# Optimization experiments

Hardware: AMD Instinct MI355X
Metric: run time of the kernel (lower is better)

The kernel has to match this reference:

```python
import jax, jax.numpy as jnp
import numpy as np
from jax import lax

B = 256; D_IN = 2048; HID = 2048; NSEG = 10; D_CTX = 1024; OUT = 100; NI = 205
KW_PCT = 0.05
K = int(round(KW_PCT * HID))  # 102 winners per sample per layer
W_DENSITY = 0.05      # weight_sparsity = 0.95
DEND_DENSITY = 0.05   # dendrite_weight_sparsity = 0.95


def setup_inputs() -> dict:
    key = jax.random.key(0)
    ks = jax.random.split(key, 16)
    def u(k, shape, bound):
        return jax.random.uniform(k, shape, minval=-bound, maxval=bound, dtype=jnp.float32)
    inp = {}
    inp["x"] = jax.random.normal(ks[0], (B, D_IN), jnp.float32)
    inp["context"] = jax.random.normal(ks[1], (B, D_CTX), jnp.float32)
    # layer 1 FF weights: modified kaiming, input density 1.0 -> bound = 1/sqrt(fan_in)
    inp["W1"] = u(ks[2], (HID, D_IN), 1.0 / np.sqrt(D_IN))
    inp["b1"] = jnp.zeros((HID,), jnp.float32)
    # dendrites: input density 1.0 (context_percent_on=1), weight density 0.05
    dend_bound = 1.0 / np.sqrt(DEND_DENSITY * D_CTX)
    inp["segW1"] = u(ks[3], (HID, NSEG, D_CTX), dend_bound)
    inp["maskW1"] = (jax.random.uniform(ks[4], (HID, D_IN)) < W_DENSITY).astype(jnp.float32)
    inp["maskS1"] = (jax.random.uniform(ks[5], (HID, NSEG, D_CTX)) < DEND_DENSITY).astype(jnp.float32)
    # layer 2 FF weights: input density = kw_percent_on (k-winners upstream)
    inp["W2"] = u(ks[6], (HID, HID), 1.0 / np.sqrt(KW_PCT * HID))
    inp["b2"] = jnp.zeros((HID,), jnp.float32)
    inp["segW2"] = u(ks[7], (HID, NSEG, D_CTX), dend_bound)
    inp["maskW2"] = (jax.random.uniform(ks[8], (HID, HID)) < W_DENSITY).astype(jnp.float32)
    inp["maskS2"] = (jax.random.uniform(ks[9], (HID, NSEG, D_CTX)) < DEND_DENSITY).astype(jnp.float32)
    # Dale (EiDense) output head: non-negative excitatory/inhibitory factors
    s = 1.0 / np.sqrt(HID)
    inp["Wex_out"] = jax.random.uniform(ks[10], (OUT, HID), dtype=jnp.float32) * s
    inp["Wix_out"] = jax.random.uniform(ks[11], (1, HID), dtype=jnp.float32) * s
    inp["Wei_out"] = jax.random.uniform(ks[12], (OUT, 1), dtype=jnp.float32)
    inp["b_out"] = jnp.zeros((OUT,), jnp.float32)
    return inp


def _kwinners(y, k):
    # keep top-k activations per row, zero the rest (boost_strength=0)
    vals, idxs = lax.top_k(y, k)  # [B, k]
    rows = jnp.arange(y.shape[0])[:, None]
    return jnp.zeros_like(y).at[rows, idxs].set(vals)


def _dendritic_layer(x, context, W, b, segW, maskW, maskS):
    # sparse-masked feedforward projection
    y = x @ (W * maskW).T + b  # [B, HID]
    # per-unit dendrite segment activations from context
    d = jnp.einsum('bc,usc->bus', context, segW * maskS)  # [B, HID, NSEG]
    # absolute-max gating: pick segment with max |activation|, gate by sigmoid
    sel = jnp.argmax(jnp.abs(d), axis=-1)  # [B, HID]
    chosen = jnp.take_along_axis(d, sel[..., None], axis=-1)[..., 0]
    y = y * jax.nn.sigmoid(chosen)
    return _kwinners(y, K)


def reference(x, context, W1, b1, segW1, maskW1, maskS1, W2, b2, segW2, maskW2, maskS2, Wex_out, Wix_out, Wei_out, b_out):
    h = _dendritic_layer(x, context, W1, b1, segW1, maskW1, maskS1)
    h = _dendritic_layer(h, context, W2, b2, segW2, maskW2, maskS2)
    # EiDense output head: W = Wex - Wei @ Wix (Dale's law), no output nonlinearity
    W_out = Wex_out - Wei_out @ Wix_out  # [OUT, HID]
    return h @ W_out.T + b_out
```

## Files before the change

### kernel.cpp

```cpp
#include <hip/hip_runtime.h>
#include <math.h>

#define B_SZ   256
#define D_IN   2048
#define HID    2048
#define NSEG   10
#define D_CTX  1024
#define OUT_N  100
#define KWIN   102
#define CAP    256

typedef float f32x4 __attribute__((ext_vector_type(4)));

__device__ __forceinline__ f32x4 ntld4(const float* p) {
  return __builtin_nontemporal_load((const f32x4*)p);
}

__device__ __forceinline__ unsigned f2key(float f) {
  unsigned b = __float_as_uint(f);
  return (b & 0x80000000u) ? ~b : (b | 0x80000000u);
}
__device__ __forceinline__ float key2f(unsigned k) {
  return (k & 0x80000000u) ? __uint_as_float(k & 0x7FFFFFFFu) : __uint_as_float(~k);
}

__global__ __launch_bounds__(256) void transpose_k(const float* __restrict__ src,
                                                   float* __restrict__ dst,
                                                   int rows, int cols) {
  __shared__ float tile[32][33];
  int c0 = blockIdx.x * 32, r0 = blockIdx.y * 32;
  int tx = threadIdx.x, ty = threadIdx.y;
  for (int i = ty; i < 32; i += 8)
    tile[i][tx] = src[(r0 + i) * cols + (c0 + tx)];
  __syncthreads();
  for (int i = ty; i < 32; i += 8)
    dst[(c0 + i) * rows + (r0 + tx)] = tile[tx][i];
}

__device__ __forceinline__ int compact_seg(const float* __restrict__ wrow,
                                           const float* __restrict__ mrow,
                                           int len4, float2* pairs, int* scnt) {
  const int t = threadIdx.x & 63;
  if (t == 0) *scnt = 0;
  __syncthreads();
  for (int e = t; e < len4; e += 64) {
    f32x4 w = ntld4(wrow + 4 * e);
    f32x4 m = ntld4(mrow + 4 * e);
    bool n0 = (m.x != 0.f), n1 = (m.y != 0.f), n2 = (m.z != 0.f), n3 = (m.w != 0.f);
    int nz = (int)n0 + (int)n1 + (int)n2 + (int)n3;
    if (nz) {
      int pos = atomicAdd(scnt, nz);
      int c = e << 2;
      if (n0) { if (pos < CAP) pairs[pos] = make_float2(w.x, __int_as_float(c));     pos++; }
      if (n1) { if (pos < CAP) pairs[pos] = make_float2(w.y, __int_as_float(c + 1)); pos++; }
      if (n2) { if (pos < CAP) pairs[pos] = make_float2(w.z, __int_as_float(c + 2)); pos++; }
      if (n3) { if (pos < CAP) pairs[pos] = make_float2(w.w, __int_as_float(c + 3)); pos++; }
    }
  }
  __syncthreads();
  int c = *scnt;
  return c > CAP ? CAP : c;
}

__device__ __forceinline__ void gather_dot(const float* __restrict__ src,
                                           const float2* pairs, int cnt,
                                           int t4, float out4[4]) {
  float acc[4][4];
#pragma unroll
  for (int s = 0; s < 4; ++s)
#pragma unroll
    for (int i = 0; i < 4; ++i) acc[s][i] = 0.f;
  int j = 0;
  for (; j + 8 <= cnt; j += 8) {
#pragma unroll
    for (int s = 0; s < 8; ++s) {
      float2 p = pairs[j + s];
      const f32x4 cv = *(const f32x4*)(src + (__float_as_int(p.y) << 8) + t4);
      acc[s & 3][0] += cv.x * p.x; acc[s & 3][1] += cv.y * p.x;
      acc[s & 3][2] += cv.z * p.x; acc[s & 3][3] += cv.w * p.x;
    }
  }
  for (; j < cnt; ++j) {
    float2 p = pairs[j];
    const f32x4 cv = *(const f32x4*)(src + (__float_as_int(p.y) << 8) + t4);
    acc[0][0] += cv.x * p.x; acc[0][1] += cv.y * p.x;
    acc[0][2] += cv.z * p.x; acc[0][3] += cv.w * p.x;
  }
#pragma unroll
  for (int i = 0; i < 4; ++i)
    out4[i] = (acc[0][i] + acc[1][i]) + (acc[2][i] + acc[3][i]);
}

__global__ __launch_bounds__(256, 4) void dend_kernel(
    const float* __restrict__ W1, const float* __restrict__ maskW1, const float* __restrict__ b1,
    const float* __restrict__ segW1, const float* __restrict__ maskS1,
    const float* __restrict__ segW2, const float* __restrict__ maskS2,
    const float* __restrict__ xT, const float* __restrict__ ctxT,
    float* __restrict__ y1T, float* __restrict__ gate2T) {
  __shared__ float2 pairs_s[4][CAP];
  __shared__ int scnt_s[4];
  const int wave = threadIdx.x >> 6;
  const int t = threadIdx.x & 63, t4 = t * 4;
  float2* pairs = pairs_s[wave];
  int* scnt = &scnt_s[wave];
  const int row = blockIdx.x * 4 + wave;

  float bestA[4] = {-1.f, -1.f, -1.f, -1.f};
  float chosen[4] = {0.f, 0.f, 0.f, 0.f};

  if (row < HID) {
    const int u = row;
    int cnt = compact_seg(W1 + u * D_IN, maskW1 + u * D_IN, D_IN / 4, pairs, scnt);
    float ff[4];
    gather_dot(xT, pairs, cnt, t4, ff);
    for (int s = 0; s < NSEG; ++s) {
      const int r = (u * NSEG + s) * D_CTX;
      cnt = compact_seg(segW1 + r, maskS1 + r, D_CTX / 4, pairs, scnt);
      float d[4];
      gather_dot(ctxT, pairs, cnt, t4, d);
#pragma unroll
      for (int i = 0; i < 4; ++i) {
        float a = fabsf(d[i]);
        if (a > bestA[i]) { bestA[i] = a; chosen[i] = d[i]; }
      }
    }
    float bb = b1[u];
    float4 o;
    o.x = (ff[0] + bb) / (1.f + expf(-chosen[0]));
    o.y = (ff[1] + bb) / (1.f + expf(-chosen[1]));
    o.z = (ff[2] + bb) / (1.f + expf(-chosen[2]));
    o.w = (ff[3] + bb) / (1.f + expf(-chosen[3]));
    *(float4*)(y1T + u * B_SZ + t4) = o;
  } else {
    const int u = row - HID;
    for (int s = 0; s < NSEG; ++s) {
      const int r = (u * NSEG + s) * D_CTX;
      int cnt = compact_seg(segW2 + r, maskS2 + r, D_CTX / 4, pairs, scnt);
      float d[4];
      gather_dot(ctxT, pairs, cnt, t4, d);
#pragma unroll
      for (int i = 0; i < 4; ++i) {
        float a = fabsf(d[i]);
        if (a > bestA[i]) { bestA[i] = a; chosen[i] = d[i]; }
      }
    }
    float4 g;
    g.x = 1.f / (1.f + expf(-chosen[0]));
    g.y = 1.f / (1.f + expf(-chosen[1]));
    g.z = 1.f / (1.f + expf(-chosen[2]));
    g.w = 1.f / (1.f + expf(-chosen[3]));
    *(float4*)(gate2T + u * B_SZ + t4) = g;
  }
}

__global__ __launch_bounds__(256, 4) void ff2_kernel(
    const float* __restrict__ W2, const float* __restrict__ maskW2, const float* __restrict__ b2,
    const float* __restrict__ h1T, const float* __restrict__ gate2T, float* __restrict__ y2T) {
  __shared__ float2 pairs_s[4][CAP];
  __shared__ int scnt_s[4];
  const int wave = threadIdx.x >> 6;
  const int t = threadIdx.x & 63, t4 = t * 4;
  const int u = blockIdx.x * 4 + wave;
  int cnt = compact_seg(W2 + u * HID, maskW2 + u * HID, HID / 4, pairs_s[wave], &scnt_s[wave]);
  float acc[4];
  gather_dot(h1T, pairs_s[wave], cnt, t4, acc);
  float bb = b2[u];
  float4 g = *(const float4*)(gate2T + u * B_SZ + t4);
  float4 o;
  o.x = (acc[0] + bb) * g.x; o.y = (acc[1] + bb) * g.y;
  o.z = (acc[2] + bb) * g.z; o.w = (acc[3] + bb) * g.w;
  *(float4*)(y2T + u * B_SZ + t4) = o;
}

__global__ __launch_bounds__(256) void topk_kernel(float* __restrict__ y) {
  const int b = blockIdx.x, t = threadIdx.x;
  __shared__ int hist[256];
  __shared__ int sfx[256];
  __shared__ unsigned sPref;
  __shared__ int sRem;
  float* __restrict__ row = y + b * HID;
  unsigned myk[8];
  f32x4 v0 = *(const f32x4*)(row + t * 8);
  f32x4 v1 = *(const f32x4*)(row + t * 8 + 4);
  myk[0] = f2key(v0.x); myk[1] = f2key(v0.y); myk[2] = f2key(v0.z); myk[3] = f2key(v0.w);
  myk[4] = f2key(v1.x); myk[5] = f2key(v1.y); myk[6] = f2key(v1.z); myk[7] = f2key(v1.w);
  unsigned pref = 0;
  int rem = KWIN;
  for (int shift = 24; shift >= 0; shift -= 8) {
    hist[t] = 0;
    __syncthreads();
    unsigned hiMask = (shift == 24) ? 0u : (0xFFFFFFFFu << (shift + 8));
#pragma unroll
    for (int i = 0; i < 8; ++i) {
      unsigned k = myk[i];
      if ((k & hiMask) == pref) atomicAdd(&hist[(k >> shift) & 255], 1);
    }
    __syncthreads();
    sfx[t] = hist[t];
    __syncthreads();
    for (int off = 1; off < 256; off <<= 1) {
      int add = (t + off < 256) ? sfx[t + off] : 0;
      __syncthreads();
      sfx[t] += add;
      __syncthreads();
    }
    int s_incl = sfx[t];
    int s_excl = (t == 255) ? 0 : sfx[t + 1];
    if (s_incl >= rem && s_excl < rem) {
      sPref = pref | (((unsigned)t) << shift);
      sRem = rem - s_excl;
    }
    __syncthreads();
    pref = sPref;
    rem = sRem;
    __syncthreads();
  }
  int eq = 0;
#pragma unroll
  for (int i = 0; i < 8; ++i) eq += (myk[i] == pref) ? 1 : 0;
  sfx[t] = eq;
  __syncthreads();
  for (int off = 1; off < 256; off <<= 1) {
    int add = (t >= off) ? sfx[t - off] : 0;
    __syncthreads();
    sfx[t] += add;
    __syncthreads();
  }
  int excl = sfx[t] - eq;
  int taken = 0;
  float o[8];
#pragma unroll
  for (int i = 0; i < 8; ++i) {
    unsigned k = myk[i];
    bool keep;
    if (k > pref) keep = true;
    else if (k == pref) { keep = (excl + taken) < rem; taken++; }
    else keep = false;
    o[i] = keep ? key2f(k) : 0.f;
  }
  f32x4 w0 = {o[0], o[1], o[2], o[3]};
  f32x4 w1 = {o[4], o[5], o[6], o[7]};
  *(f32x4*)(row + t * 8) = w0;
  *(f32x4*)(row + t * 8 + 4) = w1;
}

__global__ __launch_bounds__(256) void out_kernel(
    const float* __restrict__ h2, const float* __restrict__ Wex, const float* __restrict__ Wix,
    const float* __restrict__ Wei, const float* __restrict__ bo, float* __restrict__ out) {
  const int b = blockIdx.x, t = threadIdx.x;
  __shared__ float hrow[HID];
  __shared__ float red[256];
  float part = 0.f;
#pragma unroll
  for (int i = 0; i < 8; ++i) {
    int u = t + 256 * i;
    float v = h2[b * HID + u];
    hrow[u] = v;
    part += v * Wix[u];
  }
  red[t] = part;
  __syncthreads();
  for (int off = 128; off > 0; off >>= 1) {
    if (t < off) red[t] += red[t + off];
    __syncthreads();
  }
  float S = red[0];
  const int w = t >> 6, l = t & 63;
  for (int o = w; o < OUT_N; o += 4) {
    float acc = 0.f;
    const float* wr = Wex + o * HID;
#pragma unroll
    for (int q = 0; q < HID / 64; ++q) acc += hrow[l + 64 * q] * wr[l + 64 * q];
    for (int off = 32; off > 0; off >>= 1) acc += __shfl_down(acc, off, 64);
    if (l == 0) out[b * OUT_N + o] = acc - Wei[o] * S + bo[o];
  }
}

extern "C" void kernel_launch(void* const* d_in, const int* in_sizes, int n_in,
                              void* d_out, int out_size, void* d_ws, size_t ws_size,
                              hipStream_t stream) {
  const float* x      = (const float*)d_in[0];
  const float* ctx    = (const float*)d_in[1];
  const float* W1     = (const float*)d_in[2];
  const float* b1     = (const float*)d_in[3];
  const float* segW1  = (const float*)d_in[4];
  const float* maskW1 = (const float*)d_in[5];
  const float* maskS1 = (const float*)d_in[6];
  const float* W2     = (const float*)d_in[7];
  const float* b2     = (const float*)d_in[8];
  const float* segW2  = (const float*)d_in[9];
  const float* maskW2 = (const float*)d_in[10];
  const float* maskS2 = (const float*)d_in[11];
  const float* Wex    = (const float*)d_in[12];
  const float* Wix    = (const float*)d_in[13];
  const float* Wei    = (const float*)d_in[14];
  const float* bo     = (const float*)d_in[15];
  float* out = (float*)d_out;
  float* ws = (float*)d_ws;

  float* xT     = ws;
  float* ctxT   = ws + 524288;
  float* y1T    = ws + 786432;
  float* bufA   = ws + 1310720;
  float* h1T    = ws + 1835008;
  float* gate2T = ws + 2359296;

  dim3 tb(32, 8);
  transpose_k<<<dim3(D_IN / 32, B_SZ / 32), tb, 0, stream>>>(x, xT, B_SZ, D_IN);
  transpose_k<<<dim3(D_CTX / 32, B_SZ / 32), tb, 0, stream>>>(ctx, ctxT, B_SZ, D_CTX);
  dend_kernel<<<2 * HID / 4, 256, 0, stream>>>(W1, maskW1, b1, segW1, maskS1, segW2, maskS2,
                                               xT, ctxT, y1T, gate2T);
  transpose_k<<<dim3(B_SZ / 32, HID / 32), tb, 0, stream>>>(y1T, bufA, HID, B_SZ);
  topk_kernel<<<B_SZ, 256, 0, stream>>>(bufA);
  transpose_k<<<dim3(HID / 32, B_SZ / 32), tb, 0, stream>>>(bufA, h1T, B_SZ, HID);
  ff2_kernel<<<HID / 4, 256, 0, stream>>>(W2, maskW2, b2, h1T, gate2T, y1T);
  transpose_k<<<dim3(B_SZ / 32, HID / 32), tb, 0, stream>>>(y1T, bufA, HID, B_SZ);
  topk_kernel<<<B_SZ, 256, 0, stream>>>(bufA);
  out_kernel<<<B_SZ, 256, 0, stream>>>(bufA, Wex, Wix, Wei, bo, out);
}
```

Before: 519.9 us.

## Prefetch dendrite segments into registers and fold transposes into top-k

The dendrite kernel now loads the next segment's weights and masks into registers while the current segment is gathered and dotted. This overlaps global-memory latency with compute, and occupancy is lowered to 3 blocks to make room for the extra registers. Per-wave compaction uses wave barriers instead of block-wide __syncthreads. The four intermediate transpose kernels are removed: top-k reads the transposed activations with strided accesses and writes either transposed or row-major output, and the two input transposes are merged into one launch. This cuts launches and round trips through intermediate buffers, at the cost of uncoalesced strided reads and writes in top-k.

```diff
diff --git a/kernel.cpp b/kernel.cpp
--- a/kernel.cpp
+++ b/kernel.cpp
@@ -24,25 +24,33 @@
   return (k & 0x80000000u) ? __uint_as_float(k & 0x7FFFFFFFu) : __uint_as_float(~k);
 }
 
-__global__ __launch_bounds__(256) void transpose_k(const float* __restrict__ src,
-                                                   float* __restrict__ dst,
-                                                   int rows, int cols) {
+__global__ __launch_bounds__(256) void transpose2_k(const float* __restrict__ xsrc,
+                                                    float* __restrict__ xdst,
+                                                    const float* __restrict__ csrc,
+                                                    float* __restrict__ cdst) {
   __shared__ float tile[32][33];
-  int c0 = blockIdx.x * 32, r0 = blockIdx.y * 32;
-  int tx = threadIdx.x, ty = threadIdx.y;
+  int bid = blockIdx.x;
+  const float* src; float* dst; int cols;
+  const int NX = (D_IN / 32) * (B_SZ / 32);
+  if (bid < NX) { src = xsrc; dst = xdst; cols = D_IN; }
+  else { bid -= NX; src = csrc; dst = cdst; cols = D_CTX; }
+  int nbx = cols / 32;
+  int bx = bid % nbx, by = bid / nbx;
+  int c0 = bx * 32, r0 = by * 32;
+  int tx = threadIdx.x & 31, ty = threadIdx.x >> 5;
   for (int i = ty; i < 32; i += 8)
     tile[i][tx] = src[(r0 + i) * cols + (c0 + tx)];
   __syncthreads();
   for (int i = ty; i < 32; i += 8)
-    dst[(c0 + i) * rows + (r0 + tx)] = tile[tx][i];
-}
-
-__device__ __forceinline__ int compact_seg(const float* __restrict__ wrow,
-                                           const float* __restrict__ mrow,
-                                           int len4, float2* pairs, int* scnt) {
+    dst[(c0 + i) * B_SZ + (r0 + tx)] = tile[tx][i];
+}
+
+__device__ __forceinline__ int compact_wave(const float* __restrict__ wrow,
+                                            const float* __restrict__ mrow,
+                                            int len4, float2* pairs, int* scnt) {
   const int t = threadIdx.x & 63;
   if (t == 0) *scnt = 0;
-  __syncthreads();
+  __builtin_amdgcn_wave_barrier();
   for (int e = t; e < len4; e += 64) {
     f32x4 w = ntld4(wrow + 4 * e);
     f32x4 m = ntld4(mrow + 4 * e);
@@ -57,9 +65,45 @@
       if (n3) { if (pos < CAP) pairs[pos] = make_float2(w.w, __int_as_float(c + 3)); pos++; }
     }
   }
-  __syncthreads();
+  __builtin_amdgcn_wave_barrier();
   int c = *scnt;
   return c > CAP ? CAP : c;
+}
+
+__device__ __forceinline__ int store_seg(const f32x4 w[4], const f32x4 m[4],
+                                         float2* pairs, int* scnt) {
+  const int t = threadIdx.x & 63;
+  if (t == 0) *scnt = 0;
+  __builtin_amdgcn_wave_barrier();
+#pragma unroll
+  for (int i = 0; i < 4; ++i) {
+    int e = t + 64 * i;
+    f32x4 ww = w[i], mm = m[i];
+    bool n0 = (mm.x != 0.f), n1 = (mm.y != 0.f), n2 = (mm.z != 0.f), n3 = (mm.w != 0.f);
+    int nz = (int)n0 + (int)n1 + (int)n2 + (int)n3;
+    if (nz) {
+      int pos = atomicAdd(scnt, nz);
+      int c = e << 2;
+      if (n0) { if (pos < CAP) pairs[pos] = make_float2(ww.x, __int_as_float(c));     pos++; }
+      if (n1) { if (pos < CAP) pairs[pos] = make_float2(ww.y, __int_as_float(c + 1)); pos++; }
+      if (n2) { if (pos < CAP) pairs[pos] = make_float2(ww.z, __int_as_float(c + 2)); pos++; }
+      if (n3) { if (pos < CAP) pairs[pos] = make_float2(ww.w, __int_as_float(c + 3)); pos++; }
+    }
+  }
+  __builtin_amdgcn_wave_barrier();
+  int c = *scnt;
+  return c > CAP ? CAP : c;
+}
+
+__device__ __forceinline__ void load_seg(const float* __restrict__ wrow,
+                                         const float* __restrict__ mrow,
+                                         f32x4 w[4], f32x4 m[4]) {
+  const int t = threadIdx.x & 63;
+#pragma unroll
+  for (int i = 0; i < 4; ++i) {
+    w[i] = ntld4(wrow + 4 * (t + 64 * i));
+    m[i] = ntld4(mrow + 4 * (t + 64 * i));
+  }
 }
 
 __device__ __forceinline__ void gather_dot(const float* __restrict__ src,
@@ -91,7 +135,7 @@
     out4[i] = (acc[0][i] + acc[1][i]) + (acc[2][i] + acc[3][i]);
 }
 
-__global__ __launch_bounds__(256, 4) void dend_kernel(
+__global__ __launch_bounds__(256, 3) void dend_kernel(
     const float* __restrict__ W1, const float* __restrict__ maskW1, const float* __restrict__ b1,
     const float* __restrict__ segW1, const float* __restrict__ maskS1,
     const float* __restrict__ segW2, const float* __restrict__ maskS2,
@@ -105,51 +149,53 @@
   int* scnt = &scnt_s[wave];
   const int row = blockIdx.x * 4 + wave;
 
+  const bool isL1 = (row < HID);
+  const int u = isL1 ? row : (row - HID);
+  const float* segW = (isL1 ? segW1 : segW2) + (size_t)u * NSEG * D_CTX;
+  const float* maskS = (isL1 ? maskS1 : maskS2) + (size_t)u * NSEG * D_CTX;
+
   float bestA[4] = {-1.f, -1.f, -1.f, -1.f};
   float chosen[4] = {0.f, 0.f, 0.f, 0.f};
-
-  if (row < HID) {
-    const int u = row;
-    int cnt = compact_seg(W1 + u * D_IN, maskW1 + u * D_IN, D_IN / 4, pairs, scnt);
-    float ff[4];
+  float ff[4] = {0.f, 0.f, 0.f, 0.f};
+
+  f32x4 w[4], m[4];
+  if (isL1) {
+    int cnt = compact_wave(W1 + (size_t)u * D_IN, maskW1 + (size_t)u * D_IN,
+                           D_IN / 4, pairs, scnt);
+    load_seg(segW, maskS, w, m);
     gather_dot(xT, pairs, cnt, t4, ff);
-    for (int s = 0; s < NSEG; ++s) {
-      const int r = (u * NSEG + s) * D_CTX;
-      cnt = compact_seg(segW1 + r, maskS1 + r, D_CTX / 4, pairs, scnt);
-      float d[4];
-      gather_dot(ctxT, pairs, cnt, t4, d);
-#pragma unroll
-      for (int i = 0; i < 4; ++i) {
-        float a = fabsf(d[i]);
-        if (a > bestA[i]) { bestA[i] = a; chosen[i] = d[i]; }
-      }
-    }
+  } else {
+    load_seg(segW, maskS, w, m);
+  }
+
+  for (int s = 0; s < NSEG; ++s) {
+    int cnt = store_seg(w, m, pairs, scnt);
+    if (s + 1 < NSEG)
+      load_seg(segW + (s + 1) * D_CTX, maskS + (s + 1) * D_CTX, w, m);
+    float d[4];
+    gather_dot(ctxT, pairs, cnt, t4, d);
+#pragma unroll
+    for (int i = 0; i < 4; ++i) {
+      float a = fabsf(d[i]);
+      if (a > bestA[i]) { bestA[i] = a; chosen[i] = d[i]; }
+    }
+  }
+
+  if (isL1) {
     float bb = b1[u];
     float4 o;
     o.x = (ff[0] + bb) / (1.f + expf(-chosen[0]));
     o.y = (ff[1] + bb) / (1.f + expf(-chosen[1]));
     o.z = (ff[2] + bb) / (1.f + expf(-chosen[2]));
     o.w = (ff[3] + bb) / (1.f + expf(-chosen[3]));
-    *(float4*)(y1T + u * B_SZ + t4) = o;
+    *(float4*)(y1T + (size_t)u * B_SZ + t4) = o;
   } else {
-    const int u = row - HID;
-    for (int s = 0; s < NSEG; ++s) {
-      const int r = (u * NSEG + s) * D_CTX;
-      int cnt = compact_seg(segW2 + r, maskS2 + r, D_CTX / 4, pairs, scnt);
-      float d[4];
-      gather_dot(ctxT, pairs, cnt, t4, d);
-#pragma unroll
-      for (int i = 0; i < 4; ++i) {
-        float a = fabsf(d[i]);
-        if (a > bestA[i]) { bestA[i] = a; chosen[i] = d[i]; }
-      }
-    }
     float4 g;
     g.x = 1.f / (1.f + expf(-chosen[0]));
     g.y = 1.f / (1.f + expf(-chosen[1]));
     g.z = 1.f / (1.f + expf(-chosen[2]));
     g.w = 1.f / (1.f + expf(-chosen[3]));
-    *(float4*)(gate2T + u * B_SZ + t4) = g;
+    *(float4*)(gate2T + (size_t)u * B_SZ + t4) = g;
   }
 }
 
@@ -161,29 +207,29 @@
   const int wave = threadIdx.x >> 6;
   const int t = threadIdx.x & 63, t4 = t * 4;
   const int u = blockIdx.x * 4 + wave;
-  int cnt = compact_seg(W2 + u * HID, maskW2 + u * HID, HID / 4, pairs_s[wave], &scnt_s[wave]);
+  int cnt = compact_wave(W2 + (size_t)u * HID, maskW2 + (size_t)u * HID,
+                         HID / 4, pairs_s[wave], &scnt_s[wave]);
   float acc[4];
   gather_dot(h1T, pairs_s[wave], cnt, t4, acc);
   float bb = b2[u];
-  float4 g = *(const float4*)(gate2T + u * B_SZ + t4);
+  float4 g = *(const float4*)(gate2T + (size_t)u * B_SZ + t4);
   float4 o;
   o.x = (acc[0] + bb) * g.x; o.y = (acc[1] + bb) * g.y;
   o.z = (acc[2] + bb) * g.z; o.w = (acc[3] + bb) * g.w;
-  *(float4*)(y2T + u * B_SZ + t4) = o;
-}
-
-__global__ __launch_bounds__(256) void topk_kernel(float* __restrict__ y) {
+  *(float4*)(y2T + (size_t)u * B_SZ + t4) = o;
+}
+
+__global__ __launch_bounds__(256) void topk_kernel(const float* __restrict__ yT,
+                                                   float* __restrict__ dst, int mode) {
   const int b = blockIdx.x, t = threadIdx.x;
   __shared__ int hist[256];
   __shared__ int sfx[256];
   __shared__ unsigned sPref;
   __shared__ int sRem;
-  float* __restrict__ row = y + b * HID;
   unsigned myk[8];
-  f32x4 v0 = *(const f32x4*)(row + t * 8);
-  f32x4 v1 = *(const f32x4*)(row + t * 8 + 4);
-  myk[0] = f2key(v0.x); myk[1] = f2key(v0.y); myk[2] = f2key(v0.z); myk[3] = f2key(v0.w);
-  myk[4] = f2key(v1.x); myk[5] = f2key(v1.y); myk[6] = f2key(v1.z); myk[7] = f2key(v1.w);
+#pragma unroll
+  for (int i = 0; i < 8; ++i)
+    myk[i] = f2key(yT[(size_t)(t * 8 + i) * B_SZ + b]);
   unsigned pref = 0;
   int rem = KWIN;
   for (int shift = 24; shift >= 0; shift -= 8) {
@@ -228,7 +274,6 @@
   }
   int excl = sfx[t] - eq;
   int taken = 0;
-  float o[8];
 #pragma unroll
   for (int i = 0; i < 8; ++i) {
     unsigned k = myk[i];
@@ -236,12 +281,11 @@
     if (k > pref) keep = true;
     else if (k == pref) { keep = (excl + taken) < rem; taken++; }
     else keep = false;
-    o[i] = keep ? key2f(k) : 0.f;
-  }
-  f32x4 w0 = {o[0], o[1], o[2], o[3]};
-  f32x4 w1 = {o[4], o[5], o[6], o[7]};
-  *(f32x4*)(row + t * 8) = w0;
-  *(f32x4*)(row + t * 8 + 4) = w1;
+    float f = keep ? key2f(k) : 0.f;
+    int uu = t * 8 + i;
+    if (mode == 0) dst[(size_t)uu * B_SZ + b] = f;
+    else dst[(size_t)b * HID + uu] = f;
+  }
 }
 
 __global__ __launch_bounds__(256) void out_kernel(
@@ -254,7 +298,7 @@
 #pragma unroll
   for (int i = 0; i < 8; ++i) {
     int u = t + 256 * i;
-    float v = h2[b * HID + u];
+    float v = h2[(size_t)b * HID + u];
     hrow[u] = v;
     part += v * Wix[u];
   }
@@ -268,11 +312,11 @@
   const int w = t >> 6, l = t & 63;
   for (int o = w; o < OUT_N; o += 4) {
     float acc = 0.f;
-    const float* wr = Wex + o * HID;
+    const float* wr = Wex + (size_t)o * HID;
 #pragma unroll
     for (int q = 0; q < HID / 64; ++q) acc += hrow[l + 64 * q] * wr[l + 64 * q];
     for (int off = 32; off > 0; off >>= 1) acc += __shfl_down(acc, off, 64);
-    if (l == 0) out[b * OUT_N + o] = acc - Wei[o] * S + bo[o];
+    if (l == 0) out[(size_t)b * OUT_N + o] = acc - Wei[o] * S + bo[o];
   }
 }
 
@@ -301,20 +345,15 @@
   float* xT     = ws;
   float* ctxT   = ws + 524288;
   float* y1T    = ws + 786432;
-  float* bufA   = ws + 1310720;
-  float* h1T    = ws + 1835008;
-  float* gate2T = ws + 2359296;
-
-  dim3 tb(32, 8);
-  transpose_k<<<dim3(D_IN / 32, B_SZ / 32), tb, 0, stream>>>(x, xT, B_SZ, D_IN);
-  transpose_k<<<dim3(D_CTX / 32, B_SZ / 32), tb, 0, stream>>>(ctx, ctxT, B_SZ, D_CTX);
+  float* gate2T = ws + 1310720;
+  float* y2T    = ws + 1835008;
+  float* h2     = ws + 2359296;
+
+  transpose2_k<<<768, 256, 0, stream>>>(x, xT, ctx, ctxT);
   dend_kernel<<<2 * HID / 4, 256, 0, stream>>>(W1, maskW1, b1, segW1, maskS1, segW2, maskS2,
                                                xT, ctxT, y1T, gate2T);
-  transpose_k<<<dim3(B_SZ / 32, HID / 32), tb, 0, stream>>>(y1T, bufA, HID, B_SZ);
-  topk_kernel<<<B_SZ, 256, 0, stream>>>(bufA);
-  transpose_k<<<dim3(HID / 32, B_SZ / 32), tb, 0, stream>>>(bufA, h1T, B_SZ, HID);
-  ff2_kernel<<<HID / 4, 256, 0, stream>>>(W2, maskW2, b2, h1T, gate2T, y1T);
-  transpose_k<<<dim3(B_SZ / 32, HID / 32), tb, 0, stream>>>(y1T, bufA, HID, B_SZ);
-  topk_kernel<<<B_SZ, 256, 0, stream>>>(bufA);
-  out_kernel<<<B_SZ, 256, 0, stream>>>(bufA, Wex, Wix, Wei, bo, out);
-}
+  topk_kernel<<<B_SZ, 256, 0, stream>>>(y1T, y1T, 0);
+  ff2_kernel<<<HID / 4, 256, 0, stream>>>(W2, maskW2, b2, y1T, gate2T, y2T);
+  topk_kernel<<<B_SZ, 256, 0, stream>>>(y2T, h2, 1);
+  out_kernel<<<B_SZ, 256, 0, stream>>>(h2, Wex, Wix, Wei, bo, out);
+}
```

Result: faster. 496.0 us (-4.6%).
